# Kernel optimization log

Measured on AMD Instinct MI355X. Metric: run time of the kernel, lower is better.

The kernel has to match this reference:

```python
import jax, jax.numpy as jnp
import numpy as np

HEADS = 16
GRID_SIZE = 5      # efficient-KAN default
SPLINE_ORDER = 3   # efficient-KAN default


def _grid(in_features, dtype):
    # grid_range = [-1, 1]
    h = 2.0 / GRID_SIZE
    g = jnp.arange(-SPLINE_ORDER, GRID_SIZE + SPLINE_ORDER + 1, dtype=dtype) * h - 1.0
    return jnp.broadcast_to(g, (in_features, g.shape[0]))  # (in, G)


def _b_splines(x, grid):
    # x: (N, in), grid: (in, G); Cox-de Boor recursion
    xg = x[:, :, None]
    bases = ((xg >= grid[:, :-1]) & (xg < grid[:, 1:])).astype(x.dtype)
    for k in range(1, SPLINE_ORDER + 1):
        bases = ((xg - grid[:, :-(k + 1)]) / (grid[:, k:-1] - grid[:, :-(k + 1)]) * bases[:, :, :-1]
                 + (grid[:, k + 1:] - xg) / (grid[:, k + 1:] - grid[:, 1:-k]) * bases[:, :, 1:])
    return bases  # (N, in, GRID_SIZE + SPLINE_ORDER)


def _kan_linear(x, base_w, spline_w, spline_scaler):
    grid = _grid(x.shape[-1], x.dtype)
    base = jax.nn.silu(x) @ base_w.T                      # (N, out)
    b = _b_splines(x, grid)                               # (N, in, K)
    sw = spline_w * spline_scaler[..., None]              # (out, in, K)
    return base + jnp.einsum('nik,oik->no', b, sw)


def setup_inputs():
    key = jax.random.key(0)
    S, H = 2048, 1024
    hd = H // HEADS
    K = GRID_SIZE + SPLINE_ORDER
    ks = jax.random.split(key, 6)
    x = jax.random.normal(ks[0], (S, H), jnp.float32)
    base_w = jax.random.normal(ks[1], (3 * H, H), jnp.float32) / np.float32(np.sqrt(H))
    spline_w = jax.random.normal(ks[2], (3 * H, H, K), jnp.float32) * 0.1
    spline_scaler = 1.0 + 0.1 * jax.random.normal(ks[3], (3 * H, H), jnp.float32)
    out_w = jax.random.normal(ks[4], (H, H), jnp.float32) / np.float32(np.sqrt(H))
    out_b = jnp.zeros((H,), jnp.float32)
    # RoPE rotation matrix (unit complex), theta = 10000
    t = jnp.arange(S, dtype=jnp.float32)
    freqs = 1.0 / (10000.0 ** (jnp.arange(0, hd, 2, dtype=jnp.float32) / hd))
    ang = jnp.outer(t, freqs)  # (S, hd//2)
    return {"x": x, "base_w": base_w, "spline_w": spline_w,
            "spline_scaler": spline_scaler, "out_w": out_w, "out_b": out_b,
            "rot_cos": jnp.cos(ang), "rot_sin": jnp.sin(ang)}


def reference(x, base_w, spline_w, spline_scaler, out_w, out_b, rot_cos, rot_sin):
    S, H = x.shape
    hd = H // HEADS
    qkv = _kan_linear(x, base_w, spline_w, spline_scaler)          # (S, 3H)
    qkv = qkv.reshape(1, S, HEADS, 3 * hd).transpose(0, 2, 1, 3)   # (1,h,S,3d)
    q, k, v = jnp.split(qkv, 3, axis=-1)                           # each (1,h,S,d)

    def rope(t):
        tp = t.reshape(1, HEADS, S, hd // 2, 2)
        c = rot_cos[None, None]
        s = rot_sin[None, None]
        re = tp[..., 0] * c - tp[..., 1] * s
        im = tp[..., 0] * s + tp[..., 1] * c
        return jnp.stack([re, im], axis=-1).reshape(1, HEADS, S, hd)

    q, k = rope(q), rope(k)
    scores = jnp.einsum('bhqd,bhkd->bhqk', q, k) / np.float32(np.sqrt(hd))
    attn = jax.nn.softmax(scores, axis=-1)
    ctx = jnp.einsum('bhqk,bhkd->bhqd', attn, v)
    ctx = ctx.transpose(0, 2, 1, 3).reshape(1, S, H)
    return ctx @ out_w.T + out_b
```

## Files before the change

kernel.cpp:

```cpp
#include <hip/hip_runtime.h>

typedef unsigned short u16;
typedef __bf16 bf16x8 __attribute__((ext_vector_type(8)));
typedef float f32x4 __attribute__((ext_vector_type(4)));

#define S_LEN 2048
#define NHEADS 16
#define HD 64
#define HDIM 1024
#define QKVN 3072
#define KAUG 9216

__device__ __forceinline__ u16 f2bf(float f) {
  union { float f; unsigned u; } v; v.f = f;
  unsigned r = v.u + 0x7fffu + ((v.u >> 16) & 1u);
  return (u16)(r >> 16);
}

typedef __attribute__((address_space(1))) const unsigned int gas_u32;
typedef __attribute__((address_space(3))) unsigned int las_u32;
__device__ __forceinline__ void gload_lds16(const void* g, void* l) {
  __builtin_amdgcn_global_load_lds((gas_u32*)g, (las_u32*)l, 16, 0, 0);
}

__global__ void prep_a_kernel(const float* __restrict__ x, u16* __restrict__ Aaug) {
  int idx = blockIdx.x * 256 + threadIdx.x;
  int n = idx >> 10, i = idx & 1023;
  float xv = x[idx];
  float sil = xv / (1.0f + __expf(-xv));
  Aaug[(size_t)n * KAUG + i] = f2bf(sil);

  float b[11];
#pragma unroll
  for (int j = 0; j < 11; ++j) {
    float t0 = 0.4f * (float)(j - 3) - 1.0f;
    float t1 = 0.4f * (float)(j - 2) - 1.0f;
    b[j] = (xv >= t0 && xv < t1) ? 1.0f : 0.0f;
  }
#pragma unroll
  for (int k = 1; k <= 3; ++k) {
    const float invk = (k == 1) ? 2.5f : (k == 2) ? 1.25f : 0.83333333f;
#pragma unroll
    for (int j = 0; j < 10; ++j) {
      if (j + k < 11) {
        float tj   = 0.4f * (float)(j - 3) - 1.0f;
        float tjk1 = 0.4f * (float)(j + k - 2) - 1.0f;
        b[j] = ((xv - tj) * b[j] + (tjk1 - xv) * b[j + 1]) * invk;
      }
    }
  }
  u16 t[8];
#pragma unroll
  for (int j = 0; j < 8; ++j) t[j] = f2bf(b[j]);
  uint4 pk;
  pk.x = (unsigned)t[0] | ((unsigned)t[1] << 16);
  pk.y = (unsigned)t[2] | ((unsigned)t[3] << 16);
  pk.z = (unsigned)t[4] | ((unsigned)t[5] << 16);
  pk.w = (unsigned)t[6] | ((unsigned)t[7] << 16);
  *reinterpret_cast<uint4*>(&Aaug[(size_t)n * KAUG + 1024 + i * 8]) = pk;
}

__global__ void prep_w_kernel(const float* __restrict__ bw, const float* __restrict__ sw,
                              const float* __restrict__ sc, u16* __restrict__ Waug) {
  int idx = blockIdx.x * 256 + threadIdx.x;
  int o = idx >> 10, i = idx & 1023;
  Waug[(size_t)o * KAUG + i] = f2bf(bw[idx]);
  float s = sc[idx];
  const float4* sp = reinterpret_cast<const float4*>(sw + (size_t)idx * 8);
  float4 a = sp[0], b = sp[1];
  uint4 pk;
  pk.x = (unsigned)f2bf(a.x * s) | ((unsigned)f2bf(a.y * s) << 16);
  pk.y = (unsigned)f2bf(a.z * s) | ((unsigned)f2bf(a.w * s) << 16);
  pk.z = (unsigned)f2bf(b.x * s) | ((unsigned)f2bf(b.y * s) << 16);
  pk.w = (unsigned)f2bf(b.z * s) | ((unsigned)f2bf(b.w * s) << 16);
  *reinterpret_cast<uint4*>(&Waug[(size_t)o * KAUG + 1024 + i * 8]) = pk;
}

__global__ void prep_ow_kernel(const float* __restrict__ ow, u16* __restrict__ owbf) {
  int idx = blockIdx.x * 256 + threadIdx.x;
  float4 v = reinterpret_cast<const float4*>(ow)[idx];
  uint2 pk;
  pk.x = (unsigned)f2bf(v.x) | ((unsigned)f2bf(v.y) << 16);
  pk.y = (unsigned)f2bf(v.z) | ((unsigned)f2bf(v.w) << 16);
  reinterpret_cast<uint2*>(owbf)[idx] = pk;
}

__global__ __launch_bounds__(256) void gemm_bt(
    const u16* __restrict__ A, const u16* __restrict__ B, float* __restrict__ C,
    int M, int N, int K, int Ksp)
{
  __shared__ u16 As[128 * 32];
  __shared__ u16 Bs[128 * 32];
  const int tid = threadIdx.x;
  const int lane = tid & 63;
  const int w = tid >> 6;
  const int wr = w >> 1, wc = w & 1;
  const int row0 = blockIdx.y * 128, col0 = blockIdx.x * 128;
  const int lr = lane & 15, lg = lane >> 4;
  const int kbeg = blockIdx.z * Ksp;
  const int nsteps = Ksp >> 5;
  float* Cz = C + (size_t)blockIdx.z * M * N;

  f32x4 acc[4][4];
#pragma unroll
  for (int m = 0; m < 4; ++m)
#pragma unroll
    for (int n = 0; n < 4; ++n) acc[m][n] = (f32x4){0.f, 0.f, 0.f, 0.f};

  const int srow = tid >> 2;
  const int kch  = (tid & 3) ^ ((srow >> 1) & 3);
  const u16* ga = A + (size_t)(row0 + srow) * K + kbeg + kch * 8;
  const u16* gb = B + (size_t)(col0 + srow) * K + kbeg + kch * 8;
  const size_t rstep = (size_t)64 * K;

  const int slotx = (lg ^ ((lr >> 1) & 3)) * 8;

  for (int ks = 0; ks < nsteps; ++ks) {
    gload_lds16(ga, &As[tid * 8]);
    gload_lds16(ga + rstep, &As[2048 + tid * 8]);
    gload_lds16(gb, &Bs[tid * 8]);
    gload_lds16(gb + rstep, &Bs[2048 + tid * 8]);
    ga += 32; gb += 32;
    __syncthreads();

    bf16x8 af[4], bf[4];
#pragma unroll
    for (int m = 0; m < 4; ++m) {
      int r = wr * 64 + m * 16 + lr;
      af[m] = *reinterpret_cast<const bf16x8*>(&As[r * 32 + slotx]);
    }
#pragma unroll
    for (int n = 0; n < 4; ++n) {
      int r = wc * 64 + n * 16 + lr;
      bf[n] = *reinterpret_cast<const bf16x8*>(&Bs[r * 32 + slotx]);
    }
#pragma unroll
    for (int m = 0; m < 4; ++m)
#pragma unroll
      for (int n = 0; n < 4; ++n)
        acc[m][n] = __builtin_amdgcn_mfma_f32_16x16x32_bf16(af[m], bf[n], acc[m][n], 0, 0, 0);
    __syncthreads();
  }

#pragma unroll
  for (int m = 0; m < 4; ++m) {
    int row = row0 + wr * 64 + m * 16 + lg * 4;
#pragma unroll
    for (int n = 0; n < 4; ++n) {
      int col = col0 + wc * 64 + n * 16 + lr;
#pragma unroll
      for (int j = 0; j < 4; ++j)
        Cz[(size_t)(row + j) * N + col] = acc[m][n][j];
    }
  }
}

__global__ void reduce4_bias_kernel(const float* __restrict__ p, const float* __restrict__ bias,
                                    float* __restrict__ out) {
  int idx = blockIdx.x * 256 + threadIdx.x;
  const float4* p4 = reinterpret_cast<const float4*>(p);
  const size_t stride4 = (size_t)2048 * 1024 / 4;
  float4 a = p4[idx], b = p4[idx + stride4], c = p4[idx + 2 * stride4], d = p4[idx + 3 * stride4];
  float4 bv = reinterpret_cast<const float4*>(bias)[idx & 255];
  float4 r;
  r.x = a.x + b.x + c.x + d.x + bv.x;
  r.y = a.y + b.y + c.y + d.y + bv.y;
  r.z = a.z + b.z + c.z + d.z + bv.z;
  r.w = a.w + b.w + c.w + d.w + bv.w;
  reinterpret_cast<float4*>(out)[idx] = r;
}

__global__ void rope_kernel(const float* __restrict__ qkv, int nsplit,
                            const float* __restrict__ rc, const float* __restrict__ rs,
                            u16* __restrict__ qro, u16* __restrict__ kro) {
  int idx = blockIdx.x * 256 + threadIdx.x;
  int h = idx >> 16;
  int rem = idx & 65535;
  int s = rem >> 5, i = rem & 31;
  size_t boff = (size_t)s * QKVN + h * 192 + 2 * i;
  const size_t zstr = (size_t)S_LEN * QKVN;
  float q0 = 0.f, q1 = 0.f, k0 = 0.f, k1 = 0.f;
  for (int z = 0; z < nsplit; ++z) {
    const float* b = qkv + z * zstr + boff;
    float2 qv = *reinterpret_cast<const float2*>(b);
    float2 kv = *reinterpret_cast<const float2*>(b + 64);
    q0 += qv.x; q1 += qv.y; k0 += kv.x; k1 += kv.y;
  }
  float c = rc[s * 32 + i], sn = rs[s * 32 + i];
  size_t ob = ((size_t)(h * S_LEN + s)) * HD + 2 * i;
  unsigned qpk = (unsigned)f2bf((q0 * c - q1 * sn) * 0.125f) |
                 ((unsigned)f2bf((q0 * sn + q1 * c) * 0.125f) << 16);
  unsigned kpk = (unsigned)f2bf(k0 * c - k1 * sn) |
                 ((unsigned)f2bf(k0 * sn + k1 * c) << 16);
  *reinterpret_cast<unsigned*>(qro + ob) = qpk;
  *reinterpret_cast<unsigned*>(kro + ob) = kpk;
}

__global__ void vtrans_kernel(const float* __restrict__ qkv, int nsplit,
                              u16* __restrict__ vT) {
  __shared__ float tile[64][65];
  int h = blockIdx.x >> 5;
  int st = blockIdx.x & 31;
  int s0 = st * 64;
  int t = threadIdx.x;
  int r = t >> 2, c4 = t & 3;
  size_t soff = (size_t)(s0 + r) * QKVN + h * 192 + 128 + c4 * 16;
  const size_t zstr = (size_t)S_LEN * QKVN;
#pragma unroll
  for (int z4 = 0; z4 < 4; ++z4) {
    float acc4[4] = {0.f, 0.f, 0.f, 0.f};
    for (int z = 0; z < nsplit; ++z) {
      float4 v = *reinterpret_cast<const float4*>(qkv + z * zstr + soff + z4 * 4);
      acc4[0] += v.x; acc4[1] += v.y; acc4[2] += v.z; acc4[3] += v.w;
    }
    tile[r][c4 * 16 + z4 * 4 + 0] = acc4[0];
    tile[r][c4 * 16 + z4 * 4 + 1] = acc4[1];
    tile[r][c4 * 16 + z4 * 4 + 2] = acc4[2];
    tile[r][c4 * 16 + z4 * 4 + 3] = acc4[3];
  }
  __syncthreads();
  int d = t >> 2, sc = t & 3;
  u16* dst = vT + ((size_t)(h * 64 + d)) * S_LEN + s0 + sc * 16;
  unsigned wv[8];
#pragma unroll
  for (int z = 0; z < 8; ++z) {
    unsigned lo = f2bf(tile[sc * 16 + 2 * z][d]);
    unsigned hi = f2bf(tile[sc * 16 + 2 * z + 1][d]);
    wv[z] = lo | (hi << 16);
  }
  *reinterpret_cast<uint4*>(dst)     = make_uint4(wv[0], wv[1], wv[2], wv[3]);
  *reinterpret_cast<uint4*>(dst + 8) = make_uint4(wv[4], wv[5], wv[6], wv[7]);
}

__global__ __launch_bounds__(256) void attn_kernel(
    const u16* __restrict__ qro, const u16* __restrict__ kro,
    const u16* __restrict__ vT, u16* __restrict__ ctxb)
{
  const int lane = threadIdx.x & 63;
  const int w = threadIdx.x >> 6;
  const int bid = (blockIdx.x & 7) * 64 + (blockIdx.x >> 3);
  const int h = bid >> 5;
  const int qt = (bid & 31) * 4 + w;
  const int lr = lane & 15, lg = lane >> 4;

  const u16* qbase = qro + ((size_t)(h * S_LEN + qt * 16 + lr)) * HD + lg * 8;
  bf16x8 qa0 = *reinterpret_cast<const bf16x8*>(qbase);
  bf16x8 qa1 = *reinterpret_cast<const bf16x8*>(qbase + 32);

  float mrow = -3.0e38f, lrow = 0.f;
  f32x4 o[4];
#pragma unroll
  for (int n = 0; n < 4; ++n) o[n] = (f32x4){0.f, 0.f, 0.f, 0.f};

  const int sA = lr + 32 * (lg & 1);
  const int sB = sA + 16;
  const bool loHalf = (lg < 2);

  const u16* kbase = kro + ((size_t)(h * S_LEN + lr)) * HD + lg * 8;
  const u16* vbase = vT + ((size_t)(h * 64 + lr)) * S_LEN + lg * 8;

  bf16x8 kc00 = *reinterpret_cast<const bf16x8*>(kbase);
  bf16x8 kc01 = *reinterpret_cast<const bf16x8*>(kbase + 32);
  bf16x8 kc10 = *reinterpret_cast<const bf16x8*>(kbase + 16 * HD);
  bf16x8 kc11 = *reinterpret_cast<const bf16x8*>(kbase + 16 * HD + 32);

  for (int kt = 0; kt < 64; ++kt) {
    const u16* vb = vbase + kt * 32;
    bf16x8 vf0 = *reinterpret_cast<const bf16x8*>(vb);
    bf16x8 vf1 = *reinterpret_cast<const bf16x8*>(vb + (size_t)16 * S_LEN);
    bf16x8 vf2 = *reinterpret_cast<const bf16x8*>(vb + (size_t)32 * S_LEN);
    bf16x8 vf3 = *reinterpret_cast<const bf16x8*>(vb + (size_t)48 * S_LEN);
    const u16* knb = kbase + (size_t)(((kt + 1) & 63) * 32) * HD;
    bf16x8 kn00 = *reinterpret_cast<const bf16x8*>(knb);
    bf16x8 kn01 = *reinterpret_cast<const bf16x8*>(knb + 32);
    bf16x8 kn10 = *reinterpret_cast<const bf16x8*>(knb + 16 * HD);
    bf16x8 kn11 = *reinterpret_cast<const bf16x8*>(knb + 16 * HD + 32);

    f32x4 s0 = (f32x4){0.f, 0.f, 0.f, 0.f};
    f32x4 s1 = (f32x4){0.f, 0.f, 0.f, 0.f};
    __builtin_amdgcn_s_setprio(1);
    s0 = __builtin_amdgcn_mfma_f32_16x16x32_bf16(kc00, qa0, s0, 0, 0, 0);
    s0 = __builtin_amdgcn_mfma_f32_16x16x32_bf16(kc01, qa1, s0, 0, 0, 0);
    s1 = __builtin_amdgcn_mfma_f32_16x16x32_bf16(kc10, qa0, s1, 0, 0, 0);
    s1 = __builtin_amdgcn_mfma_f32_16x16x32_bf16(kc11, qa1, s1, 0, 0, 0);
    __builtin_amdgcn_s_setprio(0);

    float vmax = fmaxf(fmaxf(fmaxf(s0[0], s0[1]), fmaxf(s0[2], s0[3])),
                       fmaxf(fmaxf(s1[0], s1[1]), fmaxf(s1[2], s1[3])));
    vmax = fmaxf(vmax, __shfl_xor(vmax, 16));
    vmax = fmaxf(vmax, __shfl_xor(vmax, 32));

    if (__any(vmax > mrow + 8.0f)) {
      float mnew = fmaxf(mrow, vmax);
      float al = __expf(mrow - mnew);
      float alO[4];
#pragma unroll
      for (int j = 0; j < 4; ++j) alO[j] = __shfl(al, lg * 4 + j);
#pragma unroll
      for (int n = 0; n < 4; ++n)
#pragma unroll
        for (int j = 0; j < 4; ++j) o[n][j] *= alO[j];
      lrow *= al;
      mrow = mnew;
    }

    float p[8];
#pragma unroll
    for (int j = 0; j < 4; ++j) {
      p[j]     = __expf(s0[j] - mrow);
      p[4 + j] = __expf(s1[j] - mrow);
    }
    lrow += ((p[0] + p[1]) + (p[2] + p[3])) + ((p[4] + p[5]) + (p[6] + p[7]));

    union { bf16x8 v; uint4 u; } pk_;
#pragma unroll
    for (int j = 0; j < 8; ++j) pk_.v[j] = (__bf16)p[j];

    unsigned a0 = __shfl((int)pk_.u.x, sA), a1 = __shfl((int)pk_.u.y, sA);
    unsigned a2 = __shfl((int)pk_.u.x, sB), a3 = __shfl((int)pk_.u.y, sB);
    unsigned b0 = __shfl((int)pk_.u.z, sA), b1 = __shfl((int)pk_.u.w, sA);
    unsigned b2 = __shfl((int)pk_.u.z, sB), b3 = __shfl((int)pk_.u.w, sB);
    union { uint4 u; bf16x8 v; } pa_;
    pa_.u.x = loHalf ? a0 : b0;
    pa_.u.y = loHalf ? a1 : b1;
    pa_.u.z = loHalf ? a2 : b2;
    pa_.u.w = loHalf ? a3 : b3;

    __builtin_amdgcn_s_setprio(1);
    o[0] = __builtin_amdgcn_mfma_f32_16x16x32_bf16(pa_.v, vf0, o[0], 0, 0, 0);
    o[1] = __builtin_amdgcn_mfma_f32_16x16x32_bf16(pa_.v, vf1, o[1], 0, 0, 0);
    o[2] = __builtin_amdgcn_mfma_f32_16x16x32_bf16(pa_.v, vf2, o[2], 0, 0, 0);
    o[3] = __builtin_amdgcn_mfma_f32_16x16x32_bf16(pa_.v, vf3, o[3], 0, 0, 0);
    __builtin_amdgcn_s_setprio(0);

    kc00 = kn00; kc01 = kn01; kc10 = kn10; kc11 = kn11;
  }

  lrow += __shfl_xor(lrow, 16);
  lrow += __shfl_xor(lrow, 32);
  float linv[4];
#pragma unroll
  for (int j = 0; j < 4; ++j) linv[j] = 1.0f / __shfl(lrow, lg * 4 + j);

#pragma unroll
  for (int n = 0; n < 4; ++n) {
    int col = h * 64 + n * 16 + lr;
#pragma unroll
    for (int j = 0; j < 4; ++j) {
      int row = qt * 16 + lg * 4 + j;
      ctxb[(size_t)row * HDIM + col] = f2bf(o[n][j] * linv[j]);
    }
  }
}

extern "C" void kernel_launch(void* const* d_in, const int* in_sizes, int n_in,
                              void* d_out, int out_size, void* d_ws, size_t ws_size,
                              hipStream_t stream) {
  const float* x   = (const float*)d_in[0];
  const float* bw  = (const float*)d_in[1];
  const float* sw  = (const float*)d_in[2];
  const float* ssc = (const float*)d_in[3];
  const float* ow  = (const float*)d_in[4];
  const float* ob  = (const float*)d_in[5];
  const float* rc  = (const float*)d_in[6];
  const float* rs  = (const float*)d_in[7];
  float* out = (float*)d_out;

  char* ws = (char*)d_ws;
  const size_t MNF = 25165824;
  const int splitk = 2;

  u16*   Aaug  = (u16*)(ws);
  u16*   Waug  = (u16*)(ws + 37748736);
  float* qkv   = (float*)(ws + 94371840);
  size_t qend  = 94371840 + (size_t)splitk * MNF;
  u16*   qro   = (u16*)(ws + qend);
  u16*   kro   = (u16*)(ws + qend + 4194304);
  u16*   vT    = (u16*)(ws + qend + 8388608);
  u16*   owbf  = (u16*)(ws + qend + 12582912);
  u16*   ctxb  = (u16*)(ws + 94371840);
  float* part  = (float*)(ws + 94371840 + MNF);

  prep_a_kernel<<<8192, 256, 0, stream>>>(x, Aaug);
  prep_w_kernel<<<12288, 256, 0, stream>>>(bw, sw, ssc, Waug);
  prep_ow_kernel<<<1024, 256, 0, stream>>>(ow, owbf);

  gemm_bt<<<dim3(24, 16, splitk), 256, 0, stream>>>(Aaug, Waug, qkv, 2048, 3072, 9216,
                                                    9216 / splitk);

  rope_kernel<<<4096, 256, 0, stream>>>(qkv, splitk, rc, rs, qro, kro);
  vtrans_kernel<<<512, 256, 0, stream>>>(qkv, splitk, vT);

  attn_kernel<<<512, 256, 0, stream>>>(qro, kro, vT, ctxb);

  gemm_bt<<<dim3(8, 16, 4), 256, 0, stream>>>(ctxb, owbf, part, 2048, 1024, 1024, 256);
  reduce4_bias_kernel<<<2048, 256, 0, stream>>>(part, ob, out);
}
```

Measured before the change: 506.2 us.

## Split attention over two KV halves with merge kernel; shrink GEMM N-tile to 64

```diff
diff --git a/kernel.cpp b/kernel.cpp
--- a/kernel.cpp
+++ b/kernel.cpp
@@ -10,6 +10,7 @@
 #define HDIM 1024
 #define QKVN 3072
 #define KAUG 9216
+#define PSTR 1056
 
 __device__ __forceinline__ u16 f2bf(float f) {
   union { float f; unsigned u; } v; v.f = f;
@@ -85,27 +86,27 @@
   reinterpret_cast<uint2*>(owbf)[idx] = pk;
 }
 
-__global__ __launch_bounds__(256) void gemm_bt(
+__global__ __launch_bounds__(256, 4) void gemm_bt(
     const u16* __restrict__ A, const u16* __restrict__ B, float* __restrict__ C,
     int M, int N, int K, int Ksp)
 {
   __shared__ u16 As[128 * 32];
-  __shared__ u16 Bs[128 * 32];
+  __shared__ u16 Bs[64 * 32];
   const int tid = threadIdx.x;
   const int lane = tid & 63;
   const int w = tid >> 6;
   const int wr = w >> 1, wc = w & 1;
-  const int row0 = blockIdx.y * 128, col0 = blockIdx.x * 128;
+  const int row0 = blockIdx.y * 128, col0 = blockIdx.x * 64;
   const int lr = lane & 15, lg = lane >> 4;
   const int kbeg = blockIdx.z * Ksp;
   const int nsteps = Ksp >> 5;
   float* Cz = C + (size_t)blockIdx.z * M * N;
 
-  f32x4 acc[4][4];
+  f32x4 acc[4][2];
 #pragma unroll
   for (int m = 0; m < 4; ++m)
 #pragma unroll
-    for (int n = 0; n < 4; ++n) acc[m][n] = (f32x4){0.f, 0.f, 0.f, 0.f};
+    for (int n = 0; n < 2; ++n) acc[m][n] = (f32x4){0.f, 0.f, 0.f, 0.f};
 
   const int srow = tid >> 2;
   const int kch  = (tid & 3) ^ ((srow >> 1) & 3);
@@ -119,25 +120,24 @@
     gload_lds16(ga, &As[tid * 8]);
     gload_lds16(ga + rstep, &As[2048 + tid * 8]);
     gload_lds16(gb, &Bs[tid * 8]);
-    gload_lds16(gb + rstep, &Bs[2048 + tid * 8]);
     ga += 32; gb += 32;
     __syncthreads();
 
-    bf16x8 af[4], bf[4];
+    bf16x8 af[4], bf[2];
 #pragma unroll
     for (int m = 0; m < 4; ++m) {
       int r = wr * 64 + m * 16 + lr;
       af[m] = *reinterpret_cast<const bf16x8*>(&As[r * 32 + slotx]);
     }
 #pragma unroll
-    for (int n = 0; n < 4; ++n) {
-      int r = wc * 64 + n * 16 + lr;
+    for (int n = 0; n < 2; ++n) {
+      int r = wc * 32 + n * 16 + lr;
       bf[n] = *reinterpret_cast<const bf16x8*>(&Bs[r * 32 + slotx]);
     }
 #pragma unroll
     for (int m = 0; m < 4; ++m)
 #pragma unroll
-      for (int n = 0; n < 4; ++n)
+      for (int n = 0; n < 2; ++n)
         acc[m][n] = __builtin_amdgcn_mfma_f32_16x16x32_bf16(af[m], bf[n], acc[m][n], 0, 0, 0);
     __syncthreads();
   }
@@ -146,8 +146,8 @@
   for (int m = 0; m < 4; ++m) {
     int row = row0 + wr * 64 + m * 16 + lg * 4;
 #pragma unroll
-    for (int n = 0; n < 4; ++n) {
-      int col = col0 + wc * 64 + n * 16 + lr;
+    for (int n = 0; n < 2; ++n) {
+      int col = col0 + wc * 32 + n * 16 + lr;
 #pragma unroll
       for (int j = 0; j < 4; ++j)
         Cz[(size_t)(row + j) * N + col] = acc[m][n][j];
@@ -232,15 +232,17 @@
   *reinterpret_cast<uint4*>(dst + 8) = make_uint4(wv[4], wv[5], wv[6], wv[7]);
 }
 
-__global__ __launch_bounds__(256) void attn_kernel(
+__global__ __launch_bounds__(256, 4) void attn_kernel(
     const u16* __restrict__ qro, const u16* __restrict__ kro,
-    const u16* __restrict__ vT, u16* __restrict__ ctxb)
+    const u16* __restrict__ vT, float* __restrict__ part)
 {
   const int lane = threadIdx.x & 63;
   const int w = threadIdx.x >> 6;
-  const int bid = (blockIdx.x & 7) * 64 + (blockIdx.x >> 3);
-  const int h = bid >> 5;
-  const int qt = (bid & 31) * 4 + w;
+  const int bid = (blockIdx.x & 7) * 128 + (blockIdx.x >> 3);
+  const int h = bid >> 6;
+  const int r6 = bid & 63;
+  const int kvz = r6 >> 5;
+  const int qt = (r6 & 31) * 4 + w;
   const int lr = lane & 15, lg = lane >> 4;
 
   const u16* qbase = qro + ((size_t)(h * S_LEN + qt * 16 + lr)) * HD + lg * 8;
@@ -256,33 +258,29 @@
   const int sB = sA + 16;
   const bool loHalf = (lg < 2);
 
-  const u16* kbase = kro + ((size_t)(h * S_LEN + lr)) * HD + lg * 8;
-  const u16* vbase = vT + ((size_t)(h * 64 + lr)) * S_LEN + lg * 8;
-
-  bf16x8 kc00 = *reinterpret_cast<const bf16x8*>(kbase);
-  bf16x8 kc01 = *reinterpret_cast<const bf16x8*>(kbase + 32);
-  bf16x8 kc10 = *reinterpret_cast<const bf16x8*>(kbase + 16 * HD);
-  bf16x8 kc11 = *reinterpret_cast<const bf16x8*>(kbase + 16 * HD + 32);
-
-  for (int kt = 0; kt < 64; ++kt) {
+  const u16* kbase = kro + ((size_t)(h * S_LEN + kvz * 1024 + lr)) * HD + lg * 8;
+  const u16* vbase = vT + ((size_t)(h * 64 + lr)) * S_LEN + kvz * 1024 + lg * 8;
+
+  for (int kt = 0; kt < 32; ++kt) {
     const u16* vb = vbase + kt * 32;
     bf16x8 vf0 = *reinterpret_cast<const bf16x8*>(vb);
     bf16x8 vf1 = *reinterpret_cast<const bf16x8*>(vb + (size_t)16 * S_LEN);
     bf16x8 vf2 = *reinterpret_cast<const bf16x8*>(vb + (size_t)32 * S_LEN);
     bf16x8 vf3 = *reinterpret_cast<const bf16x8*>(vb + (size_t)48 * S_LEN);
-    const u16* knb = kbase + (size_t)(((kt + 1) & 63) * 32) * HD;
-    bf16x8 kn00 = *reinterpret_cast<const bf16x8*>(knb);
-    bf16x8 kn01 = *reinterpret_cast<const bf16x8*>(knb + 32);
-    bf16x8 kn10 = *reinterpret_cast<const bf16x8*>(knb + 16 * HD);
-    bf16x8 kn11 = *reinterpret_cast<const bf16x8*>(knb + 16 * HD + 32);
+
+    const u16* kb = kbase + (size_t)(kt * 32) * HD;
+    bf16x8 k00 = *reinterpret_cast<const bf16x8*>(kb);
+    bf16x8 k01 = *reinterpret_cast<const bf16x8*>(kb + 32);
+    bf16x8 k10 = *reinterpret_cast<const bf16x8*>(kb + 16 * HD);
+    bf16x8 k11 = *reinterpret_cast<const bf16x8*>(kb + 16 * HD + 32);
 
     f32x4 s0 = (f32x4){0.f, 0.f, 0.f, 0.f};
     f32x4 s1 = (f32x4){0.f, 0.f, 0.f, 0.f};
     __builtin_amdgcn_s_setprio(1);
-    s0 = __builtin_amdgcn_mfma_f32_16x16x32_bf16(kc00, qa0, s0, 0, 0, 0);
-    s0 = __builtin_amdgcn_mfma_f32_16x16x32_bf16(kc01, qa1, s0, 0, 0, 0);
-    s1 = __builtin_amdgcn_mfma_f32_16x16x32_bf16(kc10, qa0, s1, 0, 0, 0);
-    s1 = __builtin_amdgcn_mfma_f32_16x16x32_bf16(kc11, qa1, s1, 0, 0, 0);
+    s0 = __builtin_amdgcn_mfma_f32_16x16x32_bf16(k00, qa0, s0, 0, 0, 0);
+    s0 = __builtin_amdgcn_mfma_f32_16x16x32_bf16(k01, qa1, s0, 0, 0, 0);
+    s1 = __builtin_amdgcn_mfma_f32_16x16x32_bf16(k10, qa0, s1, 0, 0, 0);
+    s1 = __builtin_amdgcn_mfma_f32_16x16x32_bf16(k11, qa1, s1, 0, 0, 0);
     __builtin_amdgcn_s_setprio(0);
 
     float vmax = fmaxf(fmaxf(fmaxf(s0[0], s0[1]), fmaxf(s0[2], s0[3])),
@@ -332,25 +330,47 @@
     o[2] = __builtin_amdgcn_mfma_f32_16x16x32_bf16(pa_.v, vf2, o[2], 0, 0, 0);
     o[3] = __builtin_amdgcn_mfma_f32_16x16x32_bf16(pa_.v, vf3, o[3], 0, 0, 0);
     __builtin_amdgcn_s_setprio(0);
-
-    kc00 = kn00; kc01 = kn01; kc10 = kn10; kc11 = kn11;
   }
 
   lrow += __shfl_xor(lrow, 16);
   lrow += __shfl_xor(lrow, 32);
-  float linv[4];
-#pragma unroll
-  for (int j = 0; j < 4; ++j) linv[j] = 1.0f / __shfl(lrow, lg * 4 + j);
-
+
+  float* pb = part + (size_t)(((h * 128 + qt) * 2 + kvz)) * PSTR;
 #pragma unroll
   for (int n = 0; n < 4; ++n) {
-    int col = h * 64 + n * 16 + lr;
-#pragma unroll
-    for (int j = 0; j < 4; ++j) {
-      int row = qt * 16 + lg * 4 + j;
-      ctxb[(size_t)row * HDIM + col] = f2bf(o[n][j] * linv[j]);
-    }
-  }
+    int col = n * 16 + lr;
+#pragma unroll
+    for (int j = 0; j < 4; ++j)
+      pb[(lg * 4 + j) * 64 + col] = o[n][j];
+  }
+  if (lane < 16) {
+    pb[1024 + lr] = mrow;
+    pb[1040 + lr] = lrow;
+  }
+}
+
+__global__ void attn_merge_kernel(const float* __restrict__ part, u16* __restrict__ ctxb) {
+  int t = threadIdx.x;
+  int hq = blockIdx.x;
+  int h = hq >> 7, qt = hq & 127;
+  int row = t >> 4, c0 = (t & 15) * 4;
+  const float* p0 = part + (size_t)(hq * 2) * PSTR;
+  const float* p1 = p0 + PSTR;
+  float m0 = p0[1024 + row], l0 = p0[1040 + row];
+  float m1 = p1[1024 + row], l1 = p1[1040 + row];
+  float mx = fmaxf(m0, m1);
+  float w0 = __expf(m0 - mx), w1 = __expf(m1 - mx);
+  float inv = 1.0f / (l0 * w0 + l1 * w1);
+  const float* o0 = p0 + row * 64 + c0;
+  const float* o1 = p1 + row * 64 + c0;
+  u16 ov[4];
+#pragma unroll
+  for (int j = 0; j < 4; ++j)
+    ov[j] = f2bf((o0[j] * w0 + o1[j] * w1) * inv);
+  uint2 pk;
+  pk.x = (unsigned)ov[0] | ((unsigned)ov[1] << 16);
+  pk.y = (unsigned)ov[2] | ((unsigned)ov[3] << 16);
+  *reinterpret_cast<uint2*>(ctxb + (size_t)(qt * 16 + row) * HDIM + h * 64 + c0) = pk;
 }
 
 extern "C" void kernel_launch(void* const* d_in, const int* in_sizes, int n_in,
@@ -378,21 +398,23 @@
   u16*   kro   = (u16*)(ws + qend + 4194304);
   u16*   vT    = (u16*)(ws + qend + 8388608);
   u16*   owbf  = (u16*)(ws + qend + 12582912);
-  u16*   ctxb  = (u16*)(ws + 94371840);
-  float* part  = (float*)(ws + 94371840 + MNF);
+  float* apart = (float*)(ws + 94371840);
+  u16*   ctxb  = (u16*)(ws + 119537664);
+  float* part  = (float*)(ws + 123731968);
 
   prep_a_kernel<<<8192, 256, 0, stream>>>(x, Aaug);
   prep_w_kernel<<<12288, 256, 0, stream>>>(bw, sw, ssc, Waug);
   prep_ow_kernel<<<1024, 256, 0, stream>>>(ow, owbf);
 
-  gemm_bt<<<dim3(24, 16, splitk), 256, 0, stream>>>(Aaug, Waug, qkv, 2048, 3072, 9216,
+  gemm_bt<<<dim3(48, 16, splitk), 256, 0, stream>>>(Aaug, Waug, qkv, 2048, 3072, 9216,
                                                     9216 / splitk);
 
   rope_kernel<<<4096, 256, 0, stream>>>(qkv, splitk, rc, rs, qro, kro);
   vtrans_kernel<<<512, 256, 0, stream>>>(qkv, splitk, vT);
 
-  attn_kernel<<<512, 256, 0, stream>>>(qro, kro, vT, ctxb);
-
-  gemm_bt<<<dim3(8, 16, 4), 256, 0, stream>>>(ctxb, owbf, part, 2048, 1024, 1024, 256);
+  attn_kernel<<<1024, 256, 0, stream>>>(qro, kro, vT, apart);
+  attn_merge_kernel<<<2048, 256, 0, stream>>>(apart, ctxb);
+
+  gemm_bt<<<dim3(16, 16, 4), 256, 0, stream>>>(ctxb, owbf, part, 2048, 1024, 1024, 256);
   reduce4_bias_kernel<<<2048, 256, 0, stream>>>(part, ob, out);
 }
```

Result: slower. 559.4 us (+10.5%).
